# Kernel optimization log

Measured on AMD Instinct MI355X. Metric: run time of the kernel, lower is better.

## Reference

```python
import jax, jax.numpy as jnp
import numpy as np
from jax.ops import segment_sum

N = 100000
E = 1600000
NFEAT = 512
NHID = 256
NCLASS = 64
K = 8
ALPHA = 0.1
NEG_SLOPE = 0.2


def setup_inputs() -> dict:
    key = jax.random.key(0)
    ks = jax.random.split(key, 16)
    x = jax.random.normal(ks[0], (N, NFEAT), dtype=jnp.float32)
    src = jax.random.randint(ks[1], (E,), 0, N)
    dst = jax.random.randint(ks[2], (E,), 0, N)
    weights = jax.random.uniform(ks[3], (E, 1), dtype=jnp.float32)
    latp = jax.random.normal(ks[4], (N, NCLASS), dtype=jnp.float32) * 0.1
    W_in = jax.random.normal(ks[5], (NFEAT, NHID), dtype=jnp.float32) * (1.0 / np.sqrt(NFEAT))
    W_out = jax.random.normal(ks[6], (NHID, NCLASS), dtype=jnp.float32) * (1.0 / np.sqrt(NHID))
    Ws1 = jax.random.normal(ks[7], (NCLASS, NCLASS), dtype=jnp.float32) * (1.0 / np.sqrt(NCLASS))
    b1 = jnp.zeros((NCLASS,), dtype=jnp.float32)
    Ws2 = jax.random.normal(ks[8], (NCLASS, NCLASS), dtype=jnp.float32) * (1.0 / np.sqrt(NCLASS))
    b2 = jnp.zeros((NCLASS,), dtype=jnp.float32)
    attn_l = jax.random.normal(ks[9], (1, NCLASS), dtype=jnp.float32) * 0.1
    attn_r = jax.random.normal(ks[10], (1, NCLASS), dtype=jnp.float32) * 0.1
    s_attn = jax.random.normal(ks[11], (1, NCLASS), dtype=jnp.float32) * 0.1
    beta = jnp.zeros((1, 1), dtype=jnp.float32)
    theta = jnp.zeros((1, 1), dtype=jnp.float32)
    aw = jax.random.normal(ks[12], (1, 2), dtype=jnp.float32) * 0.1
    return {"x": x, "src": src, "dst": dst, "weights": weights, "latp": latp,
            "W_in": W_in, "W_out": W_out, "Ws1": Ws1, "b1": b1, "Ws2": Ws2, "b2": b2,
            "attn_l": attn_l, "attn_r": attn_r, "s_attn": s_attn,
            "beta": beta, "theta": theta, "aw": aw}


def reference(x, src, dst, weights, latp, W_in, W_out, Ws1, b1, Ws2, b2,
              attn_l, attn_r, s_attn, beta, theta, aw):
    # node MLP (dropout is identity in eval mode)
    h = jax.nn.elu(x @ W_in) @ W_out                      # [N, nclass]
    # position MLP on latp
    hl = jax.nn.elu(latp @ Ws1 + b1)
    hl = jax.nn.elu(hl @ Ws2 + b2)                        # [N, nclass]

    # edge attention scores
    lr = jax.nn.leaky_relu(h, NEG_SLOPE)
    el = jnp.sum(lr * attn_l, axis=-1)                    # [N]
    er = jnp.sum(lr * attn_r, axis=-1)                    # [N]
    e = el[src] + er[dst]                                 # [E]
    se = jnp.sum((hl * s_attn)[src] * hl[dst], axis=-1)   # [E]
    e = e + se

    # divergence terms
    sdf = jnp.sum((h[src] - h[dst]) ** 2, axis=-1)        # [E]
    sds = jnp.sum((hl[src] - hl[dst]) ** 2, axis=-1)      # [E]
    wt = jax.nn.softmax(aw, axis=1)
    d = wt[0, 0] * sdf + wt[0, 1] * sds

    betaw = 2.0 / (jnp.exp(-beta[0, 0]) + 1.0)
    ew = jnp.exp(e - betaw * d) + 1e-9                    # [E]

    # symmetric ('both') edge-weight normalization
    deg_src = segment_sum(ew, src, num_segments=N)        # out-degree weight sums
    deg_dst = segment_sum(ew, dst, num_segments=N)        # in-degree weight sums
    w = (deg_src ** -0.5)[src] * (deg_dst ** -0.5)[dst] * ew
    perm = 1e-9 / (jnp.exp(-theta[0, 0]) + 1.0)           # WL perturbation
    w = w + perm                                          # [E]

    # k-step weighted propagation
    feat0 = h
    fp = h
    wcol = w[:, None]
    for _ in range(K):
        agg = segment_sum(fp[src] * wcol, dst, num_segments=N)
        fp = (1.0 - ALPHA) * agg + ALPHA * feat0

    # position loss
    lp_loss = jnp.sum(hl[src] * weights * hl[dst])

    out = jax.nn.log_softmax(jax.nn.elu(fp), axis=1)
    return out, lp_loss
```

## Files before the change

### kernel.cpp

```cpp
#include <hip/hip_runtime.h>
#include <math.h>

#define NN 100000
#define EE 1600000
#define NFEATC 512
#define NHIDC 256
#define NCC 64
#define ALPHA_C 0.1f
#define NSLOPE_C 0.2f
#define SCAN_NB ((NN + 255) / 256)

typedef __attribute__((ext_vector_type(8))) short short8;
typedef __attribute__((ext_vector_type(4))) short short4v;
typedef __attribute__((ext_vector_type(4))) float floatx4;

__device__ __forceinline__ short f2bf(float f) {
    unsigned u = __float_as_uint(f);
    unsigned r = (u + 0x7FFFu + ((u >> 16) & 1u)) >> 16;
    return (short)r;
}
__device__ __forceinline__ float bf2f(short s) {
    return __uint_as_float(((unsigned)(unsigned short)s) << 16);
}

__global__ __launch_bounds__(256)
void castWT_kernel(const float* __restrict__ W, short* __restrict__ WT, int K, int Ncols)
{
    int k = blockIdx.x;
    int n = threadIdx.x;
    if (k < K && n < Ncols)
        WT[(size_t)n * K + k] = f2bf(W[(size_t)k * Ncols + n]);
}

__global__ __launch_bounds__(256)
void cast_bf_kernel(const float* __restrict__ in, short* __restrict__ out, int n4)
{
    int i = blockIdx.x * 256 + threadIdx.x;
    if (i >= n4) return;
    float4 v = reinterpret_cast<const float4*>(in)[i];
    short4v o;
    o[0] = f2bf(v.x); o[1] = f2bf(v.y); o[2] = f2bf(v.z); o[3] = f2bf(v.w);
    reinterpret_cast<short4v*>(out)[i] = o;
}

__global__ __launch_bounds__(256)
void gemm1_mfma_kernel(const float* __restrict__ x, const short* __restrict__ WT,
                       float* __restrict__ h1, int M)
{
    __shared__ short As[128][40];
    __shared__ short Bs[256][40];
    const int tid = threadIdx.x;
    const int bm = blockIdx.x * 128;
    const int wave = tid >> 6;
    const int lane = tid & 63;
    const int wm = wave >> 1;
    const int wn = wave & 1;
    const int l16 = lane & 15;
    const int quad = lane >> 4;

    floatx4 acc[4][8];
    #pragma unroll
    for (int i = 0; i < 4; ++i)
        #pragma unroll
        for (int j = 0; j < 8; ++j)
            acc[i][j] = (floatx4){0.f, 0.f, 0.f, 0.f};

    const int ar = tid >> 1;
    const int ah = tid & 1;
    const int xrow = bm + ar;
    const float* xp = x + (size_t)xrow * NFEATC + ah * 16;
    const short* wp = WT + (size_t)tid * NFEATC;

    for (int kt = 0; kt < NFEATC; kt += 32) {
        float4 a0, a1, a2, a3;
        if (xrow < M) {
            a0 = *reinterpret_cast<const float4*>(xp + kt + 0);
            a1 = *reinterpret_cast<const float4*>(xp + kt + 4);
            a2 = *reinterpret_cast<const float4*>(xp + kt + 8);
            a3 = *reinterpret_cast<const float4*>(xp + kt + 12);
        } else {
            a0 = a1 = a2 = a3 = make_float4(0.f, 0.f, 0.f, 0.f);
        }
        const short8* wq = reinterpret_cast<const short8*>(wp + kt);
        short8 b0 = wq[0], b1 = wq[1], b2 = wq[2], b3 = wq[3];

        short8 s0, s1;
        s0[0] = f2bf(a0.x); s0[1] = f2bf(a0.y); s0[2] = f2bf(a0.z); s0[3] = f2bf(a0.w);
        s0[4] = f2bf(a1.x); s0[5] = f2bf(a1.y); s0[6] = f2bf(a1.z); s0[7] = f2bf(a1.w);
        s1[0] = f2bf(a2.x); s1[1] = f2bf(a2.y); s1[2] = f2bf(a2.z); s1[3] = f2bf(a2.w);
        s1[4] = f2bf(a3.x); s1[5] = f2bf(a3.y); s1[6] = f2bf(a3.z); s1[7] = f2bf(a3.w);

        __syncthreads();
        *reinterpret_cast<short8*>(&As[ar][ah * 16 + 0]) = s0;
        *reinterpret_cast<short8*>(&As[ar][ah * 16 + 8]) = s1;
        *reinterpret_cast<short8*>(&Bs[tid][0])  = b0;
        *reinterpret_cast<short8*>(&Bs[tid][8])  = b1;
        *reinterpret_cast<short8*>(&Bs[tid][16]) = b2;
        *reinterpret_cast<short8*>(&Bs[tid][24]) = b3;
        __syncthreads();

        short8 af[4], bfr[8];
        #pragma unroll
        for (int mi = 0; mi < 4; ++mi)
            af[mi] = *reinterpret_cast<const short8*>(&As[wm * 64 + mi * 16 + l16][quad * 8]);
        #pragma unroll
        for (int ni = 0; ni < 8; ++ni)
            bfr[ni] = *reinterpret_cast<const short8*>(&Bs[wn * 128 + ni * 16 + l16][quad * 8]);
        #pragma unroll
        for (int mi = 0; mi < 4; ++mi)
            #pragma unroll
            for (int ni = 0; ni < 8; ++ni)
                acc[mi][ni] = __builtin_amdgcn_mfma_f32_16x16x32_bf16(af[mi], bfr[ni], acc[mi][ni], 0, 0, 0);
    }

    #pragma unroll
    for (int mi = 0; mi < 4; ++mi) {
        #pragma unroll
        for (int r = 0; r < 4; ++r) {
            int row = bm + wm * 64 + mi * 16 + quad * 4 + r;
            if (row >= M) continue;
            float* outp = h1 + (size_t)row * NHIDC + wn * 128 + l16;
            #pragma unroll
            for (int ni = 0; ni < 8; ++ni) {
                float v = acc[mi][ni][r];
                v = (v > 0.f) ? v : (expf(v) - 1.f);
                outp[ni * 16] = v;
            }
        }
    }
}

template<int ACT>
__global__ __launch_bounds__(256)
void gemm_kernel(const float* __restrict__ A, const float* __restrict__ B,
                 const float* __restrict__ bias, float* __restrict__ C,
                 int M, int K, int Ncols)
{
    __shared__ float As[16][68];
    __shared__ float Bs[16][64];
    const int tid = threadIdx.x;
    const int bm = blockIdx.x * 64;
    const int bn = blockIdx.y * 64;
    const int m0 = (tid & 15) * 4;
    const int n0 = (tid >> 4) * 4;
    float acc[4][4] = {};

    const int am = bm + (tid >> 2);
    const int ak = (tid & 3) * 4;
    const int bk = tid >> 4;
    const int bn4 = bn + (tid & 15) * 4;

    for (int kt = 0; kt < K; kt += 16) {
        float4 av;
        if (am < M) av = *reinterpret_cast<const float4*>(A + (size_t)am * K + kt + ak);
        else        av = make_float4(0.f, 0.f, 0.f, 0.f);
        float4 bv = *reinterpret_cast<const float4*>(B + (size_t)(kt + bk) * Ncols + bn4);
        __syncthreads();
        As[ak + 0][tid >> 2] = av.x;
        As[ak + 1][tid >> 2] = av.y;
        As[ak + 2][tid >> 2] = av.z;
        As[ak + 3][tid >> 2] = av.w;
        *reinterpret_cast<float4*>(&Bs[bk][(tid & 15) * 4]) = bv;
        __syncthreads();
        #pragma unroll
        for (int k = 0; k < 16; ++k) {
            float4 a4 = *reinterpret_cast<const float4*>(&As[k][m0]);
            float4 b4 = *reinterpret_cast<const float4*>(&Bs[k][n0]);
            float a_[4] = {a4.x, a4.y, a4.z, a4.w};
            float b_[4] = {b4.x, b4.y, b4.z, b4.w};
            #pragma unroll
            for (int i = 0; i < 4; ++i)
                #pragma unroll
                for (int j = 0; j < 4; ++j)
                    acc[i][j] = fmaf(a_[i], b_[j], acc[i][j]);
        }
    }

    float bvals[4] = {0.f, 0.f, 0.f, 0.f};
    if (bias) {
        bvals[0] = bias[bn + n0 + 0]; bvals[1] = bias[bn + n0 + 1];
        bvals[2] = bias[bn + n0 + 2]; bvals[3] = bias[bn + n0 + 3];
    }
    #pragma unroll
    for (int i = 0; i < 4; ++i) {
        int r = bm + m0 + i;
        if (r >= M) break;
        float v[4];
        #pragma unroll
        for (int j = 0; j < 4; ++j) {
            float t = acc[i][j] + bvals[j];
            if (ACT == 1) t = (t > 0.f) ? t : (expf(t) - 1.f);
            v[j] = t;
        }
        float4 o = make_float4(v[0], v[1], v[2], v[3]);
        *reinterpret_cast<float4*>(C + (size_t)r * Ncols + bn + n0) = o;
    }
}

__global__ __launch_bounds__(256)
void attn2_kernel(const float* __restrict__ h, const float* __restrict__ hl,
                  const float* __restrict__ attn_l, const float* __restrict__ attn_r,
                  const float* __restrict__ beta, const float* __restrict__ aw,
                  float* __restrict__ A, float* __restrict__ B)
{
    int node = blockIdx.x * 4 + (threadIdx.x >> 6);
    int lane = threadIdx.x & 63;
    if (node >= NN) return;
    float v = h[(size_t)node * 64 + lane];
    float u = hl[(size_t)node * 64 + lane];
    float lr = (v > 0.f) ? v : NSLOPE_C * v;
    float a = lr * attn_l[lane];
    float b = lr * attn_r[lane];
    float nh = v * v;
    float nl = u * u;
    #pragma unroll
    for (int m = 1; m < 64; m <<= 1) {
        a += __shfl_xor(a, m);
        b += __shfl_xor(b, m);
        nh += __shfl_xor(nh, m);
        nl += __shfl_xor(nl, m);
    }
    if (lane == 0) {
        float betaw = 2.f / (expf(-beta[0]) + 1.f);
        float a0 = aw[0], a1 = aw[1];
        float mxw = fmaxf(a0, a1);
        float e0 = expf(a0 - mxw), e1 = expf(a1 - mxw);
        float inv = 1.f / (e0 + e1);
        float t = betaw * (e0 * inv * nh + e1 * inv * nl);
        A[node] = a - t;
        B[node] = b - t;
    }
}

__global__ __launch_bounds__(256)
void count_kernel(const int* __restrict__ dst, int* __restrict__ cnt)
{
    int e = blockIdx.x * 256 + threadIdx.x;
    if (e < EE) atomicAdd(cnt + dst[e], 1);
}

__global__ __launch_bounds__(256)
void scan1_kernel(const int* __restrict__ cnt, int* __restrict__ partials)
{
    int i = blockIdx.x * 256 + threadIdx.x;
    int v = (i < NN) ? cnt[i] : 0;
    #pragma unroll
    for (int m = 1; m < 64; m <<= 1) v += __shfl_xor(v, m);
    __shared__ int sred[4];
    if ((threadIdx.x & 63) == 0) sred[threadIdx.x >> 6] = v;
    __syncthreads();
    if (threadIdx.x == 0)
        partials[blockIdx.x] = sred[0] + sred[1] + sred[2] + sred[3];
}

__global__ __launch_bounds__(512)
void scan2_kernel(int* __restrict__ partials)
{
    __shared__ int s[512];
    int t = threadIdx.x;
    int v = (t < SCAN_NB) ? partials[t] : 0;
    s[t] = v;
    __syncthreads();
    #pragma unroll
    for (int off = 1; off < 512; off <<= 1) {
        int add = (t >= off) ? s[t - off] : 0;
        __syncthreads();
        s[t] += add;
        __syncthreads();
    }
    if (t < SCAN_NB) partials[t] = s[t] - v;
}

__global__ __launch_bounds__(256)
void scan3_kernel(const int* __restrict__ cnt, const int* __restrict__ partials,
                  int* __restrict__ row, int* __restrict__ cur)
{
    __shared__ int s[256];
    int t = threadIdx.x;
    int i = blockIdx.x * 256 + t;
    int v = (i < NN) ? cnt[i] : 0;
    s[t] = v;
    __syncthreads();
    #pragma unroll
    for (int off = 1; off < 256; off <<= 1) {
        int add = (t >= off) ? s[t - off] : 0;
        __syncthreads();
        s[t] += add;
        __syncthreads();
    }
    int r = partials[blockIdx.x] + s[t] - v;
    if (i < NN) { row[i] = r; cur[i] = r; }
    if (i == NN - 1) row[NN] = r + v;
}

__global__ __launch_bounds__(256)
void bucket_kernel(const int* __restrict__ src, const int* __restrict__ dst,
                   const float* __restrict__ wts, int* __restrict__ cur,
                   int* __restrict__ csr_src, float* __restrict__ csr_wts)
{
    int e = blockIdx.x * 256 + threadIdx.x;
    if (e >= EE) return;
    int d = dst[e];
    int pos = atomicAdd(cur + d, 1);
    csr_src[pos] = src[e];
    csr_wts[pos] = wts[e];
}

__global__ __launch_bounds__(256)
void edge2_kernel(const int* __restrict__ row, const int* __restrict__ csr_src,
                  const float* __restrict__ csr_wts,
                  const float* __restrict__ h, const float* __restrict__ hl,
                  const float* __restrict__ A, const float* __restrict__ B,
                  const float* __restrict__ s_attn, const float* __restrict__ beta,
                  const float* __restrict__ aw,
                  float* __restrict__ ew, float* __restrict__ deg_s,
                  float* __restrict__ deg_d, float* __restrict__ lp_part)
{
    int node = blockIdx.x * 4 + (threadIdx.x >> 6);
    int lane = threadIdx.x & 63;
    int sub = lane >> 4;
    int f = lane & 15;
    float lp_p = 0.f;
    if (node < NN) {
        int b = row[node], en = row[node + 1];
        float betaw = 2.f / (expf(-beta[0]) + 1.f);
        float a0 = aw[0], a1 = aw[1];
        float mxw = fmaxf(a0, a1);
        float e0 = expf(a0 - mxw), e1 = expf(a1 - mxw);
        float inv = 1.f / (e0 + e1);
        float c0 = 2.f * betaw * e0 * inv;
        float c1 = 2.f * betaw * e1 * inv;
        const float4 hd = *reinterpret_cast<const float4*>(h  + (size_t)node * 64 + f * 4);
        const float4 ld = *reinterpret_cast<const float4*>(hl + (size_t)node * 64 + f * 4);
        const float4 sa = *reinterpret_cast<const float4*>(s_attn + f * 4);
        float4 P = make_float4(c0 * hd.x, c0 * hd.y, c0 * hd.z, c0 * hd.w);
        float4 Q = make_float4(sa.x * ld.x, sa.y * ld.y, sa.z * ld.z, sa.w * ld.w);
        float Bd = B[node];
        float degd = 0.f;
        int e = b + sub;
        for (; e + 4 < en; e += 8) {
            int s1 = csr_src[e];
            int s2 = csr_src[e + 4];
            const float4 hs1 = *reinterpret_cast<const float4*>(h  + (size_t)s1 * 64 + f * 4);
            const float4 ls1 = *reinterpret_cast<const float4*>(hl + (size_t)s1 * 64 + f * 4);
            const float4 hs2 = *reinterpret_cast<const float4*>(h  + (size_t)s2 * 64 + f * 4);
            const float4 ls2 = *reinterpret_cast<const float4*>(hl + (size_t)s2 * 64 + f * 4);
            float r1 = hs1.x * P.x + hs1.y * P.y + hs1.z * P.z + hs1.w * P.w
                     + ls1.x * Q.x + ls1.y * Q.y + ls1.z * Q.z + ls1.w * Q.w;
            float d31 = ls1.x * ld.x + ls1.y * ld.y + ls1.z * ld.z + ls1.w * ld.w;
            float r2 = hs2.x * P.x + hs2.y * P.y + hs2.z * P.z + hs2.w * P.w
                     + ls2.x * Q.x + ls2.y * Q.y + ls2.z * Q.z + ls2.w * Q.w;
            float d32 = ls2.x * ld.x + ls2.y * ld.y + ls2.z * ld.z + ls2.w * ld.w;
            #pragma unroll
            for (int m = 1; m < 16; m <<= 1) {
                r1  += __shfl_xor(r1, m);
                d31 += __shfl_xor(d31, m);
                r2  += __shfl_xor(r2, m);
                d32 += __shfl_xor(d32, m);
            }
            if (f == 0) {
                float v1 = expf(A[s1] + Bd + r1 + c1 * d31) + 1e-9f;
                ew[e] = v1;
                atomicAdd(deg_s + s1, v1);
                degd += v1;
                lp_p += d31 * csr_wts[e];
                float v2 = expf(A[s2] + Bd + r2 + c1 * d32) + 1e-9f;
                ew[e + 4] = v2;
                atomicAdd(deg_s + s2, v2);
                degd += v2;
                lp_p += d32 * csr_wts[e + 4];
            }
        }
        if (e < en) {
            int s1 = csr_src[e];
            const float4 hs1 = *reinterpret_cast<const float4*>(h  + (size_t)s1 * 64 + f * 4);
            const float4 ls1 = *reinterpret_cast<const float4*>(hl + (size_t)s1 * 64 + f * 4);
            float r1 = hs1.x * P.x + hs1.y * P.y + hs1.z * P.z + hs1.w * P.w
                     + ls1.x * Q.x + ls1.y * Q.y + ls1.z * Q.z + ls1.w * Q.w;
            float d31 = ls1.x * ld.x + ls1.y * ld.y + ls1.z * ld.z + ls1.w * ld.w;
            #pragma unroll
            for (int m = 1; m < 16; m <<= 1) {
                r1  += __shfl_xor(r1, m);
                d31 += __shfl_xor(d31, m);
            }
            if (f == 0) {
                float v1 = expf(A[s1] + Bd + r1 + c1 * d31) + 1e-9f;
                ew[e] = v1;
                atomicAdd(deg_s + s1, v1);
                degd += v1;
                lp_p += d31 * csr_wts[e];
            }
        }
        #pragma unroll
        for (int m = 16; m < 64; m <<= 1) degd += __shfl_xor(degd, m);
        if (lane == 0) deg_d[node] = degd;
    }
    #pragma unroll
    for (int m = 16; m < 64; m <<= 1) lp_p += __shfl_xor(lp_p, m);
    __shared__ float lred[4];
    if ((threadIdx.x & 63) == 0) lred[threadIdx.x >> 6] = lp_p;
    __syncthreads();
    if (threadIdx.x == 0) lp_part[blockIdx.x] = lred[0] + lred[1] + lred[2] + lred[3];
}

__global__ __launch_bounds__(256)
void reduce_kernel(const float* __restrict__ part, int n, float* __restrict__ out)
{
    float s = 0.f;
    for (int i = threadIdx.x; i < n; i += 256) s += part[i];
    #pragma unroll
    for (int m = 1; m < 64; m <<= 1) s += __shfl_xor(s, m);
    __shared__ float sd[4];
    if ((threadIdx.x & 63) == 0) sd[threadIdx.x >> 6] = s;
    __syncthreads();
    if (threadIdx.x == 0) out[0] = sd[0] + sd[1] + sd[2] + sd[3];
}

__global__ __launch_bounds__(256)
void wnorm_csr_kernel(const int* __restrict__ row, const int* __restrict__ csr_src,
                      const float* __restrict__ ew, const float* __restrict__ deg_s,
                      const float* __restrict__ deg_d, const float* __restrict__ theta,
                      float* __restrict__ csr_w)
{
    int node = blockIdx.x * 16 + (threadIdx.x >> 4);
    int f = threadIdx.x & 15;
    if (node >= NN) return;
    int b = row[node], en = row[node + 1];
    float perm = 1e-9f / (expf(-theta[0]) + 1.f);
    float dr = rsqrtf(deg_d[node]);
    for (int e = b + f; e < en; e += 16) {
        float v = ew[e] * rsqrtf(deg_s[csr_src[e]]) * dr + perm;
        csr_w[e] = (1.0f - ALPHA_C) * v;
    }
}

template<int FINAL>
__global__ __launch_bounds__(256)
void prop_kernel(const short* __restrict__ fin, const float* __restrict__ h,
                 const int* __restrict__ row, const int* __restrict__ csr_src,
                 const float* __restrict__ csr_w,
                 short* __restrict__ foutb, float* __restrict__ outf)
{
    int node = blockIdx.x * 4 + (threadIdx.x >> 6);
    int lane = threadIdx.x & 63;
    int sub = lane >> 3;
    int f = lane & 7;
    if (node >= NN) return;
    int b = row[node], en = row[node + 1];
    float acc[8] = {};
    int e = b + sub;
    for (; e + 8 < en; e += 16) {
        int s1 = csr_src[e];
        float w1 = csr_w[e];
        int s2 = csr_src[e + 8];
        float w2 = csr_w[e + 8];
        short8 v1 = *reinterpret_cast<const short8*>(fin + (size_t)s1 * 64 + f * 8);
        short8 v2 = *reinterpret_cast<const short8*>(fin + (size_t)s2 * 64 + f * 8);
        #pragma unroll
        for (int i = 0; i < 8; ++i)
            acc[i] = fmaf(w1, bf2f(v1[i]), acc[i]);
        #pragma unroll
        for (int i = 0; i < 8; ++i)
            acc[i] = fmaf(w2, bf2f(v2[i]), acc[i]);
    }
    if (e < en) {
        int s1 = csr_src[e];
        float w1 = csr_w[e];
        short8 v1 = *reinterpret_cast<const short8*>(fin + (size_t)s1 * 64 + f * 8);
        #pragma unroll
        for (int i = 0; i < 8; ++i)
            acc[i] = fmaf(w1, bf2f(v1[i]), acc[i]);
    }
    #pragma unroll
    for (int m = 8; m < 64; m <<= 1)
        #pragma unroll
        for (int i = 0; i < 8; ++i)
            acc[i] += __shfl_xor(acc[i], m);
    if (sub == 0) {
        const float4 h0 = *reinterpret_cast<const float4*>(h + (size_t)node * 64 + f * 8 + 0);
        const float4 h1v = *reinterpret_cast<const float4*>(h + (size_t)node * 64 + f * 8 + 4);
        float o[8];
        o[0] = fmaf(ALPHA_C, h0.x, acc[0]);
        o[1] = fmaf(ALPHA_C, h0.y, acc[1]);
        o[2] = fmaf(ALPHA_C, h0.z, acc[2]);
        o[3] = fmaf(ALPHA_C, h0.w, acc[3]);
        o[4] = fmaf(ALPHA_C, h1v.x, acc[4]);
        o[5] = fmaf(ALPHA_C, h1v.y, acc[5]);
        o[6] = fmaf(ALPHA_C, h1v.z, acc[6]);
        o[7] = fmaf(ALPHA_C, h1v.w, acc[7]);
        if (!FINAL) {
            short8 ob;
            #pragma unroll
            for (int i = 0; i < 8; ++i) ob[i] = f2bf(o[i]);
            *reinterpret_cast<short8*>(foutb + (size_t)node * 64 + f * 8) = ob;
        } else {
            float ev[8];
            #pragma unroll
            for (int i = 0; i < 8; ++i)
                ev[i] = (o[i] > 0.f) ? o[i] : (expf(o[i]) - 1.f);
            float mx = ev[0];
            #pragma unroll
            for (int i = 1; i < 8; ++i) mx = fmaxf(mx, ev[i]);
            #pragma unroll
            for (int m = 1; m < 8; m <<= 1) mx = fmaxf(mx, __shfl_xor(mx, m));
            float s = 0.f;
            #pragma unroll
            for (int i = 0; i < 8; ++i) s += expf(ev[i] - mx);
            #pragma unroll
            for (int m = 1; m < 8; m <<= 1) s += __shfl_xor(s, m);
            float ls = mx + logf(s);
            float4 o0 = make_float4(ev[0] - ls, ev[1] - ls, ev[2] - ls, ev[3] - ls);
            float4 o1 = make_float4(ev[4] - ls, ev[5] - ls, ev[6] - ls, ev[7] - ls);
            *reinterpret_cast<float4*>(outf + (size_t)node * 64 + f * 8 + 0) = o0;
            *reinterpret_cast<float4*>(outf + (size_t)node * 64 + f * 8 + 4) = o1;
        }
    }
}

extern "C" void kernel_launch(void* const* d_in, const int* in_sizes, int n_in,
                              void* d_out, int out_size, void* d_ws, size_t ws_size,
                              hipStream_t stream)
{
    const float* x      = (const float*)d_in[0];
    const int*   src    = (const int*)d_in[1];
    const int*   dst    = (const int*)d_in[2];
    const float* wts    = (const float*)d_in[3];
    const float* latp   = (const float*)d_in[4];
    const float* W_in   = (const float*)d_in[5];
    const float* W_out  = (const float*)d_in[6];
    const float* Ws1    = (const float*)d_in[7];
    const float* b1     = (const float*)d_in[8];
    const float* Ws2    = (const float*)d_in[9];
    const float* b2     = (const float*)d_in[10];
    const float* attn_l = (const float*)d_in[11];
    const float* attn_r = (const float*)d_in[12];
    const float* s_attn = (const float*)d_in[13];
    const float* beta   = (const float*)d_in[14];
    const float* theta  = (const float*)d_in[15];
    const float* aw     = (const float*)d_in[16];

    float* out = (float*)d_out;
    float* lp  = out + (size_t)NN * 64;

    char* w8 = (char*)d_ws;
    size_t off = 0;
    auto alloc = [&](size_t bytes) -> char* {
        char* p = w8 + off;
        off += (bytes + 255) / 256 * 256;
        return p;
    };
    float* big     = (float*)alloc((size_t)NN * 256 * 4);
    float* h1      = big;
    float* hl_tmp  = big;
    short* h_bf    = (short*)big;
    short* fpA_bf  = (short*)big + (size_t)NN * 64;
    short* fpB_bf  = (short*)big + (size_t)NN * 64 * 2;
    float* csr_wts = (float*)((short*)big + (size_t)NN * 64 * 3);
    float* h      = (float*)alloc((size_t)NN * 64 * 4);
    float* hl     = (float*)alloc((size_t)NN * 64 * 4);
    float* ew     = (float*)alloc((size_t)EE * 4);
    float* Aarr   = (float*)alloc((size_t)NN * 4);
    float* Barr   = (float*)alloc((size_t)NN * 4);
    float* deg_s  = (float*)alloc((size_t)NN * 4);
    float* deg_d  = (float*)alloc((size_t)NN * 4);
    int*   cnt    = (int*)alloc((size_t)NN * 4);
    int*   row    = (int*)alloc((size_t)(NN + 1) * 4);
    int*   cur    = (int*)alloc((size_t)NN * 4);
    int*   csr_src= (int*)alloc((size_t)EE * 4);
    float* csr_w  = (float*)alloc((size_t)EE * 4);
    float* lp_part= (float*)alloc((size_t)100000 * 4);
    int*   partials=(int*)alloc((size_t)SCAN_NB * 4);
    short* WT     = (short*)alloc((size_t)NHIDC * NFEATC * 2);

    hipMemsetAsync(cnt,   0, (size_t)NN * 4, stream);
    hipMemsetAsync(deg_s, 0, (size_t)NN * 4, stream);

    const int MB = (NN + 63) / 64;

    castWT_kernel<<<NFEATC, 256, 0, stream>>>(W_in, WT, NFEATC, NHIDC);
    gemm1_mfma_kernel<<<(NN + 127) / 128, 256, 0, stream>>>(x, WT, h1, NN);

    gemm_kernel<0><<<dim3(MB, 1), 256, 0, stream>>>(h1, W_out, nullptr, h, NN, NHIDC, NCC);
    gemm_kernel<1><<<dim3(MB, 1), 256, 0, stream>>>(latp, Ws1, b1, hl_tmp, NN, NCC, NCC);
    gemm_kernel<1><<<dim3(MB, 1), 256, 0, stream>>>(hl_tmp, Ws2, b2, hl, NN, NCC, NCC);

    attn2_kernel<<<NN / 4, 256, 0, stream>>>(h, hl, attn_l, attn_r, beta, aw, Aarr, Barr);
    count_kernel<<<EE / 256, 256, 0, stream>>>(dst, cnt);
    scan1_kernel<<<SCAN_NB, 256, 0, stream>>>(cnt, partials);
    scan2_kernel<<<1, 512, 0, stream>>>(partials);
    scan3_kernel<<<SCAN_NB, 256, 0, stream>>>(cnt, partials, row, cur);
    bucket_kernel<<<EE / 256, 256, 0, stream>>>(src, dst, wts, cur, csr_src, csr_wts);

    edge2_kernel<<<NN / 4, 256, 0, stream>>>(row, csr_src, csr_wts, h, hl, Aarr, Barr,
                                             s_attn, beta, aw, ew, deg_s, deg_d, lp_part);
    reduce_kernel<<<1, 256, 0, stream>>>(lp_part, NN / 4, lp);

    wnorm_csr_kernel<<<NN / 16, 256, 0, stream>>>(row, csr_src, ew, deg_s, deg_d, theta, csr_w);

    cast_bf_kernel<<<(NN * 64 / 4 + 255) / 256, 256, 0, stream>>>(h, h_bf, NN * 64 / 4);

    const short* fin = h_bf;
    short* bufs[2] = {fpA_bf, fpB_bf};
    for (int it = 0; it < 7; ++it) {
        short* fo = bufs[it & 1];
        prop_kernel<0><<<NN / 4, 256, 0, stream>>>(fin, h, row, csr_src, csr_w, fo, nullptr);
        fin = fo;
    }
    prop_kernel<1><<<NN / 4, 256, 0, stream>>>(fin, h, row, csr_src, csr_w, nullptr, out);
}
```

Baseline: 1.257 ms.

## Pre-swizzle W_in for direct MFMA loads, double-buffer A tile, halve prop node width

The weight cast now writes W_in in an MFMA-fragment-ready layout, so gemm1 reads B fragments straight from global memory and drops its B shared-memory staging. The A tile is double-buffered in shared memory, with the next x chunk prefetched into registers while MFMAs run, which cuts the loop to one barrier per iteration. Separately, the propagation kernel now gives each node 32 lanes instead of 64, so one block covers 8 nodes. That matches the roughly 16 edges per node and shortens the shuffle reduction. The risks are heavier global/L2 traffic for the B fragments and fewer edges processed in flight per node.

```diff
diff --git a/kernel.cpp b/kernel.cpp
--- a/kernel.cpp
+++ b/kernel.cpp
@@ -24,12 +24,14 @@
 }
 
 __global__ __launch_bounds__(256)
-void castWT_kernel(const float* __restrict__ W, short* __restrict__ WT, int K, int Ncols)
+void castWT_kernel(const float* __restrict__ W, short* __restrict__ WB)
 {
     int k = blockIdx.x;
-    int n = threadIdx.x;
-    if (k < K && n < Ncols)
-        WT[(size_t)n * K + k] = f2bf(W[(size_t)k * Ncols + n]);
+    int col = threadIdx.x;
+    short v = f2bf(W[(size_t)k * NHIDC + col]);
+    size_t idx = ((size_t)(k >> 5) * 16 + (col >> 4)) * 512
+               + (size_t)((k >> 3) & 3) * 128 + (col & 15) * 8 + (k & 7);
+    WB[idx] = v;
 }
 
 __global__ __launch_bounds__(256)
@@ -44,11 +46,10 @@
 }
 
 __global__ __launch_bounds__(256)
-void gemm1_mfma_kernel(const float* __restrict__ x, const short* __restrict__ WT,
+void gemm1_mfma_kernel(const float* __restrict__ x, const short* __restrict__ WB,
                        float* __restrict__ h1, int M)
 {
-    __shared__ short As[128][40];
-    __shared__ short Bs[256][40];
+    __shared__ short As[2][128][40];
     const int tid = threadIdx.x;
     const int bm = blockIdx.x * 128;
     const int wave = tid >> 6;
@@ -68,50 +69,61 @@
     const int ar = tid >> 1;
     const int ah = tid & 1;
     const int xrow = bm + ar;
+    const bool arow_ok = (xrow < M);
     const float* xp = x + (size_t)xrow * NFEATC + ah * 16;
-    const short* wp = WT + (size_t)tid * NFEATC;
-
-    for (int kt = 0; kt < NFEATC; kt += 32) {
-        float4 a0, a1, a2, a3;
-        if (xrow < M) {
-            a0 = *reinterpret_cast<const float4*>(xp + kt + 0);
-            a1 = *reinterpret_cast<const float4*>(xp + kt + 4);
-            a2 = *reinterpret_cast<const float4*>(xp + kt + 8);
-            a3 = *reinterpret_cast<const float4*>(xp + kt + 12);
-        } else {
-            a0 = a1 = a2 = a3 = make_float4(0.f, 0.f, 0.f, 0.f);
-        }
-        const short8* wq = reinterpret_cast<const short8*>(wp + kt);
-        short8 b0 = wq[0], b1 = wq[1], b2 = wq[2], b3 = wq[3];
-
-        short8 s0, s1;
-        s0[0] = f2bf(a0.x); s0[1] = f2bf(a0.y); s0[2] = f2bf(a0.z); s0[3] = f2bf(a0.w);
-        s0[4] = f2bf(a1.x); s0[5] = f2bf(a1.y); s0[6] = f2bf(a1.z); s0[7] = f2bf(a1.w);
-        s1[0] = f2bf(a2.x); s1[1] = f2bf(a2.y); s1[2] = f2bf(a2.z); s1[3] = f2bf(a2.w);
-        s1[4] = f2bf(a3.x); s1[5] = f2bf(a3.y); s1[6] = f2bf(a3.z); s1[7] = f2bf(a3.w);
-
-        __syncthreads();
-        *reinterpret_cast<short8*>(&As[ar][ah * 16 + 0]) = s0;
-        *reinterpret_cast<short8*>(&As[ar][ah * 16 + 8]) = s1;
-        *reinterpret_cast<short8*>(&Bs[tid][0])  = b0;
-        *reinterpret_cast<short8*>(&Bs[tid][8])  = b1;
-        *reinterpret_cast<short8*>(&Bs[tid][16]) = b2;
-        *reinterpret_cast<short8*>(&Bs[tid][24]) = b3;
-        __syncthreads();
-
-        short8 af[4], bfr[8];
+    const short* wbp = WB + (size_t)(wn * 8) * 512 + lane * 8;
+
+    float4 a0, a1, a2, a3;
+
+#define LOADA(kt)                                                         \
+    if (arow_ok) {                                                        \
+        a0 = *reinterpret_cast<const float4*>(xp + (kt) + 0);             \
+        a1 = *reinterpret_cast<const float4*>(xp + (kt) + 4);             \
+        a2 = *reinterpret_cast<const float4*>(xp + (kt) + 8);             \
+        a3 = *reinterpret_cast<const float4*>(xp + (kt) + 12);            \
+    } else {                                                              \
+        a0 = a1 = a2 = a3 = make_float4(0.f, 0.f, 0.f, 0.f);             \
+    }
+
+#define CVTSTORE(buf)                                                     \
+    {                                                                     \
+        short8 s0, s1;                                                    \
+        s0[0] = f2bf(a0.x); s0[1] = f2bf(a0.y); s0[2] = f2bf(a0.z); s0[3] = f2bf(a0.w); \
+        s0[4] = f2bf(a1.x); s0[5] = f2bf(a1.y); s0[6] = f2bf(a1.z); s0[7] = f2bf(a1.w); \
+        s1[0] = f2bf(a2.x); s1[1] = f2bf(a2.y); s1[2] = f2bf(a2.z); s1[3] = f2bf(a2.w); \
+        s1[4] = f2bf(a3.x); s1[5] = f2bf(a3.y); s1[6] = f2bf(a3.z); s1[7] = f2bf(a3.w); \
+        *reinterpret_cast<short8*>(&As[buf][ar][ah * 16 + 0]) = s0;       \
+        *reinterpret_cast<short8*>(&As[buf][ar][ah * 16 + 8]) = s1;       \
+    }
+
+    LOADA(0);
+    CVTSTORE(0);
+    LOADA(32);
+    __syncthreads();
+
+    for (int it = 0; it < 16; ++it) {
+        const int cur = it & 1;
+        short8 af[4];
         #pragma unroll
         for (int mi = 0; mi < 4; ++mi)
-            af[mi] = *reinterpret_cast<const short8*>(&As[wm * 64 + mi * 16 + l16][quad * 8]);
+            af[mi] = *reinterpret_cast<const short8*>(&As[cur][wm * 64 + mi * 16 + l16][quad * 8]);
+        short8 bfr[8];
         #pragma unroll
         for (int ni = 0; ni < 8; ++ni)
-            bfr[ni] = *reinterpret_cast<const short8*>(&Bs[wn * 128 + ni * 16 + l16][quad * 8]);
+            bfr[ni] = *reinterpret_cast<const short8*>(wbp + ((size_t)(it * 16 + ni) << 9));
         #pragma unroll
         for (int mi = 0; mi < 4; ++mi)
             #pragma unroll
             for (int ni = 0; ni < 8; ++ni)
                 acc[mi][ni] = __builtin_amdgcn_mfma_f32_16x16x32_bf16(af[mi], bfr[ni], acc[mi][ni], 0, 0, 0);
-    }
+        if (it < 15) {
+            CVTSTORE(1 - cur);
+            if (it < 14) { LOADA((it + 2) * 32); }
+        }
+        __syncthreads();
+    }
+#undef LOADA
+#undef CVTSTORE
 
     #pragma unroll
     for (int mi = 0; mi < 4; ++mi) {
@@ -441,19 +453,19 @@
                  const float* __restrict__ csr_w,
                  short* __restrict__ foutb, float* __restrict__ outf)
 {
-    int node = blockIdx.x * 4 + (threadIdx.x >> 6);
-    int lane = threadIdx.x & 63;
-    int sub = lane >> 3;
-    int f = lane & 7;
+    int node = blockIdx.x * 8 + (threadIdx.x >> 5);
+    int l32 = threadIdx.x & 31;
+    int sub = l32 >> 3;
+    int f = l32 & 7;
     if (node >= NN) return;
     int b = row[node], en = row[node + 1];
     float acc[8] = {};
     int e = b + sub;
-    for (; e + 8 < en; e += 16) {
+    for (; e + 4 < en; e += 8) {
         int s1 = csr_src[e];
         float w1 = csr_w[e];
-        int s2 = csr_src[e + 8];
-        float w2 = csr_w[e + 8];
+        int s2 = csr_src[e + 4];
+        float w2 = csr_w[e + 4];
         short8 v1 = *reinterpret_cast<const short8*>(fin + (size_t)s1 * 64 + f * 8);
         short8 v2 = *reinterpret_cast<const short8*>(fin + (size_t)s2 * 64 + f * 8);
         #pragma unroll
@@ -472,7 +484,7 @@
             acc[i] = fmaf(w1, bf2f(v1[i]), acc[i]);
     }
     #pragma unroll
-    for (int m = 8; m < 64; m <<= 1)
+    for (int m = 8; m < 32; m <<= 1)
         #pragma unroll
         for (int i = 0; i < 8; ++i)
             acc[i] += __shfl_xor(acc[i], m);
@@ -570,15 +582,15 @@
     float* csr_w  = (float*)alloc((size_t)EE * 4);
     float* lp_part= (float*)alloc((size_t)100000 * 4);
     int*   partials=(int*)alloc((size_t)SCAN_NB * 4);
-    short* WT     = (short*)alloc((size_t)NHIDC * NFEATC * 2);
+    short* WB     = (short*)alloc((size_t)NHIDC * NFEATC * 2);
 
     hipMemsetAsync(cnt,   0, (size_t)NN * 4, stream);
     hipMemsetAsync(deg_s, 0, (size_t)NN * 4, stream);
 
     const int MB = (NN + 63) / 64;
 
-    castWT_kernel<<<NFEATC, 256, 0, stream>>>(W_in, WT, NFEATC, NHIDC);
-    gemm1_mfma_kernel<<<(NN + 127) / 128, 256, 0, stream>>>(x, WT, h1, NN);
+    castWT_kernel<<<NFEATC, 256, 0, stream>>>(W_in, WB);
+    gemm1_mfma_kernel<<<(NN + 127) / 128, 256, 0, stream>>>(x, WB, h1, NN);
 
     gemm_kernel<0><<<dim3(MB, 1), 256, 0, stream>>>(h1, W_out, nullptr, h, NN, NHIDC, NCC);
     gemm_kernel<1><<<dim3(MB, 1), 256, 0, stream>>>(latp, Ws1, b1, hl_tmp, NN, NCC, NCC);
@@ -603,8 +615,8 @@
     short* bufs[2] = {fpA_bf, fpB_bf};
     for (int it = 0; it < 7; ++it) {
         short* fo = bufs[it & 1];
-        prop_kernel<0><<<NN / 4, 256, 0, stream>>>(fin, h, row, csr_src, csr_w, fo, nullptr);
+        prop_kernel<0><<<NN / 8, 256, 0, stream>>>(fin, h, row, csr_src, csr_w, fo, nullptr);
         fin = fo;
     }
-    prop_kernel<1><<<NN / 4, 256, 0, stream>>>(fin, h, row, csr_src, csr_w, nullptr, out);
-}
+    prop_kernel<1><<<NN / 8, 256, 0, stream>>>(fin, h, row, csr_src, csr_w, nullptr, out);
+}
```

New measurement: 1.161 ms. -7.6%, faster.
